# Optimization experiments

Hardware: AMD Instinct MI355X
Metric: run time of the kernel (lower is better)

The kernel has to match this reference:

```python
import jax, jax.numpy as jnp
import numpy as np

B, L, D, DIN, A, V, R = 1024, 100, 256, 704, 128, 32000, 129


def setup_inputs() -> dict:
    key = jax.random.key(0)
    ks = jax.random.split(key, 18)
    s = 0.05
    inp = {
        "x": jax.random.normal(ks[0], (B, DIN), jnp.float32),
        "h0": jax.random.normal(ks[1], (B, D), jnp.float32),
        "c0": jax.random.normal(ks[2], (B, D), jnp.float32),
        "src_enc": jax.random.normal(ks[3], (B, L, D), jnp.float32),
        "src_token_ids": jax.random.randint(ks[4], (B, L), 0, V),
        "W_ih": jax.random.normal(ks[5], (4 * D, DIN), jnp.float32) * s,
        "b_ih": jax.random.normal(ks[6], (4 * D,), jnp.float32) * s,
        "W_hh": jax.random.normal(ks[7], (4 * D, D), jnp.float32) * s,
        "b_hh": jax.random.normal(ks[8], (4 * D,), jnp.float32) * s,
        "W_attn": jax.random.normal(ks[9], (D, D), jnp.float32) * s,
        "W_att_vec": jax.random.normal(ks[10], (A * 2, 2 * D), jnp.float32) * s,
        "W_ptr": jax.random.normal(ks[11], (D, D), jnp.float32) * s,
        "rule_emb": jax.random.normal(ks[12], (R, 128), jnp.float32) * s,
        "W_rule_proj": jax.random.normal(ks[13], (D, 128), jnp.float32) * s,
        "prim_emb": jax.random.normal(ks[14], (V, 128), jnp.float32) * s,
        "W_prim_proj": jax.random.normal(ks[15], (D, 128), jnp.float32) * s,
        "w_gen": jax.random.normal(ks[16], (2, D), jnp.float32) * s,
        "b_gen": jax.random.normal(ks[17], (2,), jnp.float32) * s,
    }
    # W_att_vec maps concat(h, ctx) [2D] -> ATT (=256); keep shape (256, 512)
    inp["W_att_vec"] = inp["W_att_vec"][:256]
    return inp


def reference(x, h0, c0, src_enc, src_token_ids, W_ih, b_ih, W_hh, b_hh,
              W_attn, W_att_vec, W_ptr, rule_emb, W_rule_proj,
              prim_emb, W_prim_proj, w_gen, b_gen):
    # --- LSTMCell (torch gate order i, f, g, o) ---
    gates = x @ W_ih.T + b_ih + h0 @ W_hh.T + b_hh          # [B, 4D]
    i, f, g, o = jnp.split(gates, 4, axis=-1)
    i, f, o = jax.nn.sigmoid(i), jax.nn.sigmoid(f), jax.nn.sigmoid(o)
    c = f * c0 + i * jnp.tanh(g)
    h = o * jnp.tanh(c)                                      # [B, D]

    # --- dot-product attention over source encodings ---
    enc_proj = src_enc @ W_attn.T                            # [B, L, D]
    scores = jnp.einsum('bd,bld->bl', h, enc_proj)
    alpha = jax.nn.softmax(scores, axis=-1)
    ctx = jnp.einsum('bl,bld->bd', alpha, src_enc)
    att = jnp.tanh(jnp.concatenate([h, ctx], axis=-1) @ W_att_vec.T)  # [B, 256]

    # --- apply-rule (production) readout ---
    rule_proj = rule_emb @ W_rule_proj.T                     # [R, 256]
    log_p_rule = jax.nn.log_softmax(att @ rule_proj.T, axis=-1)  # [B, R]

    # --- primitive generation readout ---
    prim_proj = prim_emb @ W_prim_proj.T                     # [V, 256]
    p_gen_prim = jax.nn.softmax(att @ prim_proj.T, axis=-1)  # [B, V]

    # --- pointer network copy distribution over source positions ---
    ptr_scores = jnp.einsum('bld,bd->bl', src_enc @ W_ptr.T, att)
    copy_p = jax.nn.softmax(ptr_scores, axis=-1)             # [B, L]

    # --- gen vs copy gate (softmax over 2, per usage in parse()) ---
    gate = jax.nn.softmax(att @ w_gen.T + b_gen, axis=-1)    # [B, 2]

    # --- combined primitive distribution: gen + scattered copy mass ---
    p_prim = gate[:, :1] * p_gen_prim                        # [B, V]
    copy_mass = gate[:, 1:] * copy_p                         # [B, L]
    bidx = jnp.arange(p_prim.shape[0])[:, None]
    p_prim = p_prim.at[bidx, src_token_ids].add(copy_mass)
    return log_p_rule, p_prim, h, c, att
```

## Files before the change

### kernel.cpp

```cpp
#include <hip/hip_runtime.h>
#include <hip/hip_bf16.h>
#include <math.h>

#define NB   1024
#define LL   100
#define DD   256
#define DINN 704
#define VV   32000
#define RR   129
#define KAV  512

typedef float f32x4 __attribute__((ext_vector_type(4)));
typedef float f32x2 __attribute__((ext_vector_type(2)));
typedef short s16x8 __attribute__((ext_vector_type(8)));
typedef unsigned short u16;

__device__ __forceinline__ float sigf(float x) { return 1.0f / (1.0f + __expf(-x)); }

__device__ __forceinline__ u16 f2bf(float f) {
    unsigned int u = __float_as_uint(f);
    u += 0x7fffu + ((u >> 16) & 1u);
    return (u16)(u >> 16);
}

__global__ __launch_bounds__(256) void k_lstm(
    const float* __restrict__ x, const float* __restrict__ h0, const float* __restrict__ c0,
    const float* __restrict__ W_ih, const float* __restrict__ b_ih,
    const float* __restrict__ W_hh, const float* __restrict__ b_hh,
    float* __restrict__ out_h, float* __restrict__ out_c)
{
    __shared__ __align__(16) float As[16][36];
    __shared__ __align__(16) float Bs[16][68];
    __shared__ __align__(16) float gsm[32][68];
    const int t = threadIdx.x;
    const int row0 = blockIdx.x * 32;
    const int dg = blockIdx.y;
    const int tr = t >> 4, tc = t & 15;
    float acc[2][4] = {};

    for (int kt = 0; kt < 60; ++kt) {
        const float* __restrict__ Asrc;
        const float* __restrict__ Bsrc;
        int lda, kb;
        if (kt < 44) { Asrc = x;  Bsrc = W_ih; lda = DINN; kb = kt * 16; }
        else         { Asrc = h0; Bsrc = W_hh; lda = DD;   kb = (kt - 44) * 16; }
        __syncthreads();
#pragma unroll
        for (int p = 0; p < 2; ++p) {
            int e = t + p * 256;
            int r = e >> 4, kk = e & 15;
            As[kk][r] = Asrc[(row0 + r) * lda + kb + kk];
        }
#pragma unroll
        for (int p = 0; p < 4; ++p) {
            int e = t + p * 256;
            int r = e >> 4, kk = e & 15;
            int n = ((r >> 4) << 8) + dg * 16 + (r & 15);
            Bs[kk][r] = Bsrc[n * lda + kb + kk];
        }
        __syncthreads();
#pragma unroll
        for (int kk = 0; kk < 16; ++kk) {
            float a0 = As[kk][tr * 2], a1 = As[kk][tr * 2 + 1];
            f32x4 b = *reinterpret_cast<const f32x4*>(&Bs[kk][tc * 4]);
#pragma unroll
            for (int i = 0; i < 4; ++i) {
                acc[0][i] = fmaf(a0, b[i], acc[0][i]);
                acc[1][i] = fmaf(a1, b[i], acc[1][i]);
            }
        }
    }
    __syncthreads();
#pragma unroll
    for (int j = 0; j < 2; ++j)
#pragma unroll
        for (int i = 0; i < 4; ++i)
            gsm[tr * 2 + j][tc * 4 + i] = acc[j][i];
    __syncthreads();

#pragma unroll
    for (int p = 0; p < 2; ++p) {
        int item = t + p * 256;
        int r = item >> 4, di = item & 15;
        int dcol = dg * 16 + di;
        float iv = gsm[r][di]      + b_ih[dcol]          + b_hh[dcol];
        float fv = gsm[r][16 + di] + b_ih[DD + dcol]     + b_hh[DD + dcol];
        float gv = gsm[r][32 + di] + b_ih[2 * DD + dcol] + b_hh[2 * DD + dcol];
        float ov = gsm[r][48 + di] + b_ih[3 * DD + dcol] + b_hh[3 * DD + dcol];
        float cprev = c0[(row0 + r) * DD + dcol];
        float cc = sigf(fv) * cprev + sigf(iv) * tanhf(gv);
        float hh = sigf(ov) * tanhf(cc);
        out_c[(row0 + r) * DD + dcol] = cc;
        out_h[(row0 + r) * DD + dcol] = hh;
    }
}

__global__ __launch_bounds__(256) void k_conv(
    const float* __restrict__ src, u16* __restrict__ dst,
    const float* __restrict__ rule_emb, const float* __restrict__ W_rule_proj,
    float* __restrict__ rule_proj,
    const float* __restrict__ W_att_vec, float* __restrict__ wt)
{
    __shared__ float re_s[128];
    __shared__ __align__(16) float tile[64][65];
    const int bx = blockIdx.x, t = threadIdx.x;

    if (bx >= 2000) {
        const int id = bx - 2000;
        const int c0 = (id >> 3) * 64;
        const int k0 = (id & 7) * 64;
        const int r = t >> 6, cc = t & 63;
#pragma unroll
        for (int p = 0; p < 16; ++p)
            tile[r + p * 4][cc] = W_att_vec[(c0 + r + p * 4) * KAV + k0 + cc];
        __syncthreads();
#pragma unroll
        for (int p = 0; p < 16; ++p)
            wt[(k0 + r + p * 4) * DD + c0 + cc] = tile[cc][r + p * 4];
        return;
    }

    if (bx < RR && t < 128) re_s[t] = rule_emb[bx * 128 + t];

    int i = (bx * 256 + t) * 8;
    f32x4 a = *reinterpret_cast<const f32x4*>(&src[i]);
    f32x4 b = *reinterpret_cast<const f32x4*>(&src[i + 4]);
    s16x8 r;
    r[0] = (short)f2bf(a[0]); r[1] = (short)f2bf(a[1]);
    r[2] = (short)f2bf(a[2]); r[3] = (short)f2bf(a[3]);
    r[4] = (short)f2bf(b[0]); r[5] = (short)f2bf(b[1]);
    r[6] = (short)f2bf(b[2]); r[7] = (short)f2bf(b[3]);
    *reinterpret_cast<s16x8*>(&dst[i]) = r;

    if (bx < RR) {
        __syncthreads();
        float acc = 0.f;
        const float* __restrict__ wr = &W_rule_proj[t * 128];
#pragma unroll 8
        for (int k = 0; k < 128; k += 4) {
            f32x4 w4 = *reinterpret_cast<const f32x4*>(&wr[k]);
            acc += w4[0] * re_s[k] + w4[1] * re_s[k + 1]
                 + w4[2] * re_s[k + 2] + w4[3] * re_s[k + 3];
        }
        rule_proj[bx * DD + t] = acc;
    }
}

__global__ __launch_bounds__(256) void k_fused(
    const float* __restrict__ src_enc, const float* __restrict__ h,
    const float* __restrict__ W_attn, const float* __restrict__ Wt,
    const float* __restrict__ rule_proj, const float* __restrict__ W_ptr,
    const float* __restrict__ W_prim_proj, const float* __restrict__ w_gen,
    const float* __restrict__ b_gen,
    float* __restrict__ att_out, float* __restrict__ log_p_rule,
    u16* __restrict__ att_bf, float* __restrict__ gate0_ws,
    float* __restrict__ copy_mass)
{
    __shared__ __align__(16) float hc_s[2 * DD];
    __shared__ __align__(16) float att_s[DD];
    __shared__ __align__(16) float part[4][DD];
    __shared__ __align__(16) float partp[4][128];
    __shared__ float sc_s[LL];
    __shared__ float al_s[LL];
    __shared__ float red_s[RR];
    __shared__ float gl_s[2];
    __shared__ float mS[2];

    const int b = blockIdx.x, t = threadIdx.x;
    const int lane = t & 63, w = t >> 6;
    const float* __restrict__ enc = src_enc + (size_t)b * LL * DD;

    hc_s[t] = h[b * DD + t];
    __syncthreads();

    {
        f32x4 p = {0.f, 0.f, 0.f, 0.f};
        const int e0 = w * 64;
#pragma unroll 4
        for (int e = e0; e < e0 + 64; ++e) {
            float hv = hc_s[e];
            f32x4 wv = *reinterpret_cast<const f32x4*>(&W_attn[e * DD + lane * 4]);
            p[0] = fmaf(hv, wv[0], p[0]); p[1] = fmaf(hv, wv[1], p[1]);
            p[2] = fmaf(hv, wv[2], p[2]); p[3] = fmaf(hv, wv[3], p[3]);
        }
        *reinterpret_cast<f32x4*>(&part[w][lane * 4]) = p;
    }
    __syncthreads();
    f32x4 hw4;
    {
        f32x4 p0 = *reinterpret_cast<const f32x4*>(&part[0][lane * 4]);
        f32x4 p1 = *reinterpret_cast<const f32x4*>(&part[1][lane * 4]);
        f32x4 p2 = *reinterpret_cast<const f32x4*>(&part[2][lane * 4]);
        f32x4 p3 = *reinterpret_cast<const f32x4*>(&part[3][lane * 4]);
        hw4[0] = (p0[0] + p1[0]) + (p2[0] + p3[0]);
        hw4[1] = (p0[1] + p1[1]) + (p2[1] + p3[1]);
        hw4[2] = (p0[2] + p1[2]) + (p2[2] + p3[2]);
        hw4[3] = (p0[3] + p1[3]) + (p2[3] + p3[3]);
    }

    for (int l = w; l < LL; l += 4) {
        f32x4 ev = *reinterpret_cast<const f32x4*>(&enc[l * DD + lane * 4]);
        float pr = hw4[0] * ev[0] + hw4[1] * ev[1] + hw4[2] * ev[2] + hw4[3] * ev[3];
#pragma unroll
        for (int m = 1; m < 64; m <<= 1) pr += __shfl_xor(pr, m);
        if (lane == 0) sc_s[l] = pr;
    }
    __syncthreads();
    if (w == 0) {
        float v0 = sc_s[lane];
        float v1 = (lane + 64 < LL) ? sc_s[lane + 64] : -1e30f;
        float m = fmaxf(v0, v1);
#pragma unroll
        for (int s = 1; s < 64; s <<= 1) m = fmaxf(m, __shfl_xor(m, s));
        float e0 = __expf(v0 - m);
        float e1 = (lane + 64 < LL) ? __expf(v1 - m) : 0.f;
        float ssum = e0 + e1;
#pragma unroll
        for (int s = 1; s < 64; s <<= 1) ssum += __shfl_xor(ssum, s);
        float inv = 1.f / ssum;
        al_s[lane] = e0 * inv;
        if (lane + 64 < LL) al_s[lane + 64] = e1 * inv;
    }
    __syncthreads();

    {
        float a0 = 0.f, a1 = 0.f, a2 = 0.f, a3 = 0.f;
        for (int l = 0; l < LL; l += 4) {
            a0 = fmaf(al_s[l],     enc[(l)     * DD + t], a0);
            a1 = fmaf(al_s[l + 1], enc[(l + 1) * DD + t], a1);
            a2 = fmaf(al_s[l + 2], enc[(l + 2) * DD + t], a2);
            a3 = fmaf(al_s[l + 3], enc[(l + 3) * DD + t], a3);
        }
        hc_s[DD + t] = (a0 + a1) + (a2 + a3);
    }
    __syncthreads();

    {
        f32x4 p = {0.f, 0.f, 0.f, 0.f};
        const int gk0 = w * 128;
#pragma unroll 4
        for (int kk = 0; kk < 128; ++kk) {
            float cv = hc_s[gk0 + kk];
            f32x4 wv = *reinterpret_cast<const f32x4*>(&Wt[(gk0 + kk) * DD + lane * 4]);
            p[0] = fmaf(cv, wv[0], p[0]); p[1] = fmaf(cv, wv[1], p[1]);
            p[2] = fmaf(cv, wv[2], p[2]); p[3] = fmaf(cv, wv[3], p[3]);
        }
        *reinterpret_cast<f32x4*>(&part[w][lane * 4]) = p;
    }
    __syncthreads();
    {
        float av = (part[0][t] + part[1][t]) + (part[2][t] + part[3][t]);
        av = tanhf(av);
        att_s[t] = av;
        att_out[b * DD + t] = av;
    }
    __syncthreads();

    {
        f32x4 p = {0.f, 0.f, 0.f, 0.f};
        const int e0 = w * 64;
#pragma unroll 4
        for (int e = e0; e < e0 + 64; ++e) {
            float av = att_s[e];
            f32x4 wv = *reinterpret_cast<const f32x4*>(&W_ptr[e * DD + lane * 4]);
            p[0] = fmaf(av, wv[0], p[0]); p[1] = fmaf(av, wv[1], p[1]);
            p[2] = fmaf(av, wv[2], p[2]); p[3] = fmaf(av, wv[3], p[3]);
        }
        *reinterpret_cast<f32x4*>(&part[w][lane * 4]) = p;
    }
    {
        float p0 = 0.f, p1 = 0.f;
        const int e0 = w * 64;
#pragma unroll 4
        for (int e = e0; e < e0 + 64; ++e) {
            float av = att_s[e];
            f32x2 wv = *reinterpret_cast<const f32x2*>(&W_prim_proj[e * 128 + lane * 2]);
            p0 = fmaf(av, wv[0], p0);
            p1 = fmaf(av, wv[1], p1);
        }
        partp[w][lane * 2]     = p0;
        partp[w][lane * 2 + 1] = p1;
    }
    if (t < RR) {
        float acc = 0.f;
        const float* __restrict__ rp = &rule_proj[t * DD];
#pragma unroll 4
        for (int d = 0; d < DD; d += 4) {
            f32x4 r4 = *reinterpret_cast<const f32x4*>(&rp[d]);
            f32x4 a4 = *reinterpret_cast<const f32x4*>(&att_s[d]);
            acc += r4[0] * a4[0] + r4[1] * a4[1] + r4[2] * a4[2] + r4[3] * a4[3];
        }
        red_s[t] = acc;
    }
    if (w < 2) {
        f32x4 a4 = *reinterpret_cast<const f32x4*>(&att_s[lane * 4]);
        f32x4 g4 = *reinterpret_cast<const f32x4*>(&w_gen[w * DD + lane * 4]);
        float p = a4[0] * g4[0] + a4[1] * g4[1] + a4[2] * g4[2] + a4[3] * g4[3];
#pragma unroll
        for (int s = 1; s < 64; s <<= 1) p += __shfl_xor(p, s);
        if (lane == 0) gl_s[w] = p + b_gen[w];
    }
    __syncthreads();

    f32x4 aw4;
    {
        f32x4 p0 = *reinterpret_cast<const f32x4*>(&part[0][lane * 4]);
        f32x4 p1 = *reinterpret_cast<const f32x4*>(&part[1][lane * 4]);
        f32x4 p2 = *reinterpret_cast<const f32x4*>(&part[2][lane * 4]);
        f32x4 p3 = *reinterpret_cast<const f32x4*>(&part[3][lane * 4]);
        aw4[0] = (p0[0] + p1[0]) + (p2[0] + p3[0]);
        aw4[1] = (p0[1] + p1[1]) + (p2[1] + p3[1]);
        aw4[2] = (p0[2] + p1[2]) + (p2[2] + p3[2]);
        aw4[3] = (p0[3] + p1[3]) + (p2[3] + p3[3]);
    }
    if (t < 128) {
        float ap = (partp[0][t] + partp[1][t]) + (partp[2][t] + partp[3][t]);
        att_bf[b * 128 + t] = f2bf(ap);
    }
    if (w == 0) {
        float v0 = red_s[lane];
        float v1 = red_s[lane + 64];
        float v2 = (lane == 0) ? red_s[128] : -1e30f;
        float m = fmaxf(fmaxf(v0, v1), v2);
#pragma unroll
        for (int s = 1; s < 64; s <<= 1) m = fmaxf(m, __shfl_xor(m, s));
        float ssum = __expf(v0 - m) + __expf(v1 - m) + ((lane == 0) ? __expf(v2 - m) : 0.f);
#pragma unroll
        for (int s = 1; s < 64; s <<= 1) ssum += __shfl_xor(ssum, s);
        if (lane == 0) { mS[0] = m; mS[1] = logf(ssum); }
    }
    __syncthreads();
    if (t < RR) log_p_rule[b * RR + t] = red_s[t] - mS[0] - mS[1];

    float g0 = gl_s[0], g1 = gl_s[1];
    float gm = fmaxf(g0, g1);
    float e0g = __expf(g0 - gm), e1g = __expf(g1 - gm);
    float gate1 = e1g / (e0g + e1g);
    if (t == 0) gate0_ws[b] = e0g / (e0g + e1g);

    for (int l = w; l < LL; l += 4) {
        f32x4 ev = *reinterpret_cast<const f32x4*>(&enc[l * DD + lane * 4]);
        float pr = aw4[0] * ev[0] + aw4[1] * ev[1] + aw4[2] * ev[2] + aw4[3] * ev[3];
#pragma unroll
        for (int m = 1; m < 64; m <<= 1) pr += __shfl_xor(pr, m);
        if (lane == 0) sc_s[l] = pr;
    }
    __syncthreads();
    if (w == 0) {
        float v0 = sc_s[lane];
        float v1 = (lane + 64 < LL) ? sc_s[lane + 64] : -1e30f;
        float m = fmaxf(v0, v1);
#pragma unroll
        for (int s = 1; s < 64; s <<= 1) m = fmaxf(m, __shfl_xor(m, s));
        float ee0 = __expf(v0 - m);
        float ee1 = (lane + 64 < LL) ? __expf(v1 - m) : 0.f;
        float ssum = ee0 + ee1;
#pragma unroll
        for (int s = 1; s < 64; s <<= 1) ssum += __shfl_xor(ssum, s);
        float inv = 1.f / ssum;
        copy_mass[b * LL + lane] = gate1 * ee0 * inv;
        if (lane + 64 < LL) copy_mass[b * LL + lane + 64] = gate1 * ee1 * inv;
    }
}

template <int PASS>
__global__ __launch_bounds__(256) void k_prim(
    const u16* __restrict__ att_bf, const u16* __restrict__ prim_bf,
    const float* __restrict__ coef, float* __restrict__ stats, float* __restrict__ p_prim)
{
    const int t = threadIdx.x;
    const int lane = t & 63, w = t >> 6;
    const int lm = lane & 15, lq = lane >> 4;
    const int colbase = blockIdx.x * 128 + (w & 1) * 64;
    const int chunk = colbase >> 6;
    const int rowblk = blockIdx.y * 256;

    s16x8 pfr[4][4];
#pragma unroll
    for (int kg = 0; kg < 4; ++kg)
#pragma unroll
        for (int mg = 0; mg < 4; ++mg)
            pfr[kg][mg] = *reinterpret_cast<const s16x8*>(
                &prim_bf[(size_t)(colbase + mg * 16 + lm) * 128 + kg * 32 + lq * 8]);

    for (int it = 0; it < 2; ++it) {
        const int rowbase = rowblk + it * 128 + (w >> 1) * 64;
        f32x4 acc[4][4] = {};
#pragma unroll
        for (int kg = 0; kg < 4; ++kg) {
            s16x8 afr[4];
#pragma unroll
            for (int ng = 0; ng < 4; ++ng)
                afr[ng] = *reinterpret_cast<const s16x8*>(
                    &att_bf[(rowbase + ng * 16 + lm) * 128 + kg * 32 + lq * 8]);
#pragma unroll
            for (int mg = 0; mg < 4; ++mg)
#pragma unroll
                for (int ng = 0; ng < 4; ++ng)
                    acc[mg][ng] = __builtin_amdgcn_mfma_f32_16x16x32_bf16(
                        pfr[kg][mg], afr[ng], acc[mg][ng], 0, 0, 0);
        }
        if (PASS == 0) {
#pragma unroll
            for (int ng = 0; ng < 4; ++ng) {
                float se = 0.f;
#pragma unroll
                for (int mg = 0; mg < 4; ++mg)
                    se += __expf(acc[mg][ng][0]) + __expf(acc[mg][ng][1])
                        + __expf(acc[mg][ng][2]) + __expf(acc[mg][ng][3]);
                se += __shfl_xor(se, 16);
                se += __shfl_xor(se, 32);
                if (lq == 0)
                    stats[chunk * NB + rowbase + ng * 16 + lm] = se;
            }
        } else {
#pragma unroll
            for (int ng = 0; ng < 4; ++ng) {
                const int arow = rowbase + ng * 16 + lm;
                const float cf = coef[arow];
                float* __restrict__ dst = &p_prim[(size_t)arow * VV + colbase + lq * 4];
#pragma unroll
                for (int mg = 0; mg < 4; ++mg) {
                    f32x4 v;
                    v[0] = cf * __expf(acc[mg][ng][0]);
                    v[1] = cf * __expf(acc[mg][ng][1]);
                    v[2] = cf * __expf(acc[mg][ng][2]);
                    v[3] = cf * __expf(acc[mg][ng][3]);
                    *reinterpret_cast<f32x4*>(&dst[mg * 16]) = v;
                }
            }
        }
    }
}

__global__ __launch_bounds__(256) void k_combine(
    const float* __restrict__ stats, const float* __restrict__ gate0_ws,
    float* __restrict__ coef)
{
    const int row = blockIdx.x * 256 + threadIdx.x;
    float s0 = 0.f, s1 = 0.f, s2 = 0.f, s3 = 0.f;
    for (int c = 0; c < 500; c += 4) {
        s0 += stats[(c)     * NB + row];
        s1 += stats[(c + 1) * NB + row];
        s2 += stats[(c + 2) * NB + row];
        s3 += stats[(c + 3) * NB + row];
    }
    coef[row] = gate0_ws[row] / ((s0 + s1) + (s2 + s3));
}

__global__ __launch_bounds__(256) void k_scatter(
    const int* __restrict__ tok, const float* __restrict__ copy_mass, float* __restrict__ p_prim)
{
    int i = blockIdx.x * 256 + threadIdx.x;
    if (i >= NB * LL) return;
    int b = i / LL;
    atomicAdd(&p_prim[(size_t)b * VV + tok[i]], copy_mass[i]);
}

extern "C" void kernel_launch(void* const* d_in, const int* in_sizes, int n_in,
                              void* d_out, int out_size, void* d_ws, size_t ws_size,
                              hipStream_t stream)
{
    const float* x         = (const float*)d_in[0];
    const float* h0        = (const float*)d_in[1];
    const float* c0        = (const float*)d_in[2];
    const float* src_enc   = (const float*)d_in[3];
    const int*   tok       = (const int*)  d_in[4];
    const float* W_ih      = (const float*)d_in[5];
    const float* b_ih      = (const float*)d_in[6];
    const float* W_hh      = (const float*)d_in[7];
    const float* b_hh      = (const float*)d_in[8];
    const float* W_attn    = (const float*)d_in[9];
    const float* W_att_vec = (const float*)d_in[10];
    const float* W_ptr     = (const float*)d_in[11];
    const float* rule_emb  = (const float*)d_in[12];
    const float* W_rule_pr = (const float*)d_in[13];
    const float* prim_emb  = (const float*)d_in[14];
    const float* W_prim_pr = (const float*)d_in[15];
    const float* w_gen     = (const float*)d_in[16];
    const float* b_gen     = (const float*)d_in[17];

    float* out    = (float*)d_out;
    float* o_logp = out;
    float* o_pp   = out + 1024 * 129;
    float* o_h    = o_pp + (size_t)1024 * 32000;
    float* o_c    = o_h + 1024 * 256;
    float* o_att  = o_c + 1024 * 256;

    float* wsf      = (float*)d_ws;
    float* ws_rp    = wsf;
    float* ws_gate  = ws_rp    + 33280;
    float* ws_cm    = ws_gate  + 1024;
    float* ws_coef  = ws_cm    + 102400;
    float* ws_stats = ws_coef  + 1024;
    float* ws_wt    = ws_stats + 512000;
    u16*   ws_attbf = (u16*)(ws_wt + 131072);
    u16*   ws_primbf= (u16*)(ws_wt + 131072 + 65536);

    k_conv<<<dim3(2032), 256, 0, stream>>>(prim_emb, ws_primbf, rule_emb, W_rule_pr,
                                           ws_rp, W_att_vec, ws_wt);
    k_lstm<<<dim3(32, 16), 256, 0, stream>>>(x, h0, c0, W_ih, b_ih, W_hh, b_hh, o_h, o_c);
    k_fused<<<dim3(1024), 256, 0, stream>>>(src_enc, o_h, W_attn, ws_wt, ws_rp, W_ptr,
                                            W_prim_pr, w_gen, b_gen,
                                            o_att, o_logp, ws_attbf, ws_gate, ws_cm);
    k_prim<0><<<dim3(250, 4), 256, 0, stream>>>(ws_attbf, ws_primbf, nullptr, ws_stats, nullptr);
    k_combine<<<dim3(4), 256, 0, stream>>>(ws_stats, ws_gate, ws_coef);
    k_prim<1><<<dim3(250, 4), 256, 0, stream>>>(ws_attbf, ws_primbf, ws_coef, nullptr, o_pp);
    k_scatter<<<dim3(400), 256, 0, stream>>>(tok, ws_cm, o_pp);
}
```

Measured before the change: 249.8 us.

## Stage source encodings once in LDS as bf16 and reuse across attention passes

Each block now loads its row's src_enc slice once, converts it to bf16 and stores it in a padded shared-memory tile. The attention-score, context and pointer-score passes read from that tile instead of re-reading global memory three times, and score computation switches from per-row wave reductions to per-thread dot products. This cuts global memory traffic in a bandwidth-bound kernel, at the cost of bf16 precision on the encoder values and a much larger LDS footprint that lowers occupancy.

```diff
diff --git a/kernel.cpp b/kernel.cpp
--- a/kernel.cpp
+++ b/kernel.cpp
@@ -9,18 +9,23 @@
 #define VV   32000
 #define RR   129
 #define KAV  512
+#define ROWU 129
 
 typedef float f32x4 __attribute__((ext_vector_type(4)));
 typedef float f32x2 __attribute__((ext_vector_type(2)));
 typedef short s16x8 __attribute__((ext_vector_type(8)));
 typedef unsigned short u16;
+typedef unsigned int u32;
 
 __device__ __forceinline__ float sigf(float x) { return 1.0f / (1.0f + __expf(-x)); }
 
 __device__ __forceinline__ u16 f2bf(float f) {
-    unsigned int u = __float_as_uint(f);
+    u32 u = __float_as_uint(f);
     u += 0x7fffu + ((u >> 16) & 1u);
     return (u16)(u >> 16);
+}
+__device__ __forceinline__ float bf2f(u16 s) {
+    return __uint_as_float(((u32)s) << 16);
 }
 
 __global__ __launch_bounds__(256) void k_lstm(
@@ -156,10 +161,11 @@
     u16* __restrict__ att_bf, float* __restrict__ gate0_ws,
     float* __restrict__ copy_mass)
 {
-    __shared__ __align__(16) float hc_s[2 * DD];
-    __shared__ __align__(16) float att_s[DD];
+    __shared__ u32 enc_u[LL * ROWU];
     __shared__ __align__(16) float part[4][DD];
     __shared__ __align__(16) float partp[4][128];
+    __shared__ __align__(16) float hc_s[2 * DD];
+    __shared__ __align__(16) float hw_s[DD];
     __shared__ float sc_s[LL];
     __shared__ float al_s[LL];
     __shared__ float red_s[RR];
@@ -171,6 +177,17 @@
     const float* __restrict__ enc = src_enc + (size_t)b * LL * DD;
 
     hc_s[t] = h[b * DD + t];
+
+#pragma unroll 5
+    for (int p = 0; p < 25; ++p) {
+        int q = p * 256 + t;
+        int l = q >> 6, dq = q & 63;
+        f32x4 ev = *reinterpret_cast<const f32x4*>(&enc[l * DD + dq * 4]);
+        u32 w0 = (u32)f2bf(ev[0]) | ((u32)f2bf(ev[1]) << 16);
+        u32 w1 = (u32)f2bf(ev[2]) | ((u32)f2bf(ev[3]) << 16);
+        enc_u[l * ROWU + dq * 2]     = w0;
+        enc_u[l * ROWU + dq * 2 + 1] = w1;
+    }
     __syncthreads();
 
     {
@@ -186,26 +203,28 @@
         *reinterpret_cast<f32x4*>(&part[w][lane * 4]) = p;
     }
     __syncthreads();
-    f32x4 hw4;
-    {
-        f32x4 p0 = *reinterpret_cast<const f32x4*>(&part[0][lane * 4]);
-        f32x4 p1 = *reinterpret_cast<const f32x4*>(&part[1][lane * 4]);
-        f32x4 p2 = *reinterpret_cast<const f32x4*>(&part[2][lane * 4]);
-        f32x4 p3 = *reinterpret_cast<const f32x4*>(&part[3][lane * 4]);
-        hw4[0] = (p0[0] + p1[0]) + (p2[0] + p3[0]);
-        hw4[1] = (p0[1] + p1[1]) + (p2[1] + p3[1]);
-        hw4[2] = (p0[2] + p1[2]) + (p2[2] + p3[2]);
-        hw4[3] = (p0[3] + p1[3]) + (p2[3] + p3[3]);
-    }
-
-    for (int l = w; l < LL; l += 4) {
-        f32x4 ev = *reinterpret_cast<const f32x4*>(&enc[l * DD + lane * 4]);
-        float pr = hw4[0] * ev[0] + hw4[1] * ev[1] + hw4[2] * ev[2] + hw4[3] * ev[3];
-#pragma unroll
-        for (int m = 1; m < 64; m <<= 1) pr += __shfl_xor(pr, m);
-        if (lane == 0) sc_s[l] = pr;
-    }
-    __syncthreads();
+    hw_s[t] = (part[0][t] + part[1][t]) + (part[2][t] + part[3][t]);
+    __syncthreads();
+
+    {
+        const int sl = ((w >> 1) << 6) + lane;
+        float sp = 0.f;
+        if (sl < LL) {
+            const u32* __restrict__ rp = enc_u + sl * ROWU + ((w & 1) << 6);
+            const float* __restrict__ hp = hw_s + ((w & 1) << 7);
+#pragma unroll 16
+            for (int k = 0; k < 64; ++k) {
+                u32 v = rp[k];
+                sp = fmaf(bf2f((u16)v),         hp[2 * k],     sp);
+                sp = fmaf(bf2f((u16)(v >> 16)), hp[2 * k + 1], sp);
+            }
+        }
+        part[w][lane] = sp;
+    }
+    __syncthreads();
+    if (t < LL) sc_s[t] = part[(t >> 6) << 1][t & 63] + part[((t >> 6) << 1) + 1][t & 63];
+    __syncthreads();
+
     if (w == 0) {
         float v0 = sc_s[lane];
         float v1 = (lane + 64 < LL) ? sc_s[lane + 64] : -1e30f;
@@ -224,15 +243,24 @@
     __syncthreads();
 
     {
-        float a0 = 0.f, a1 = 0.f, a2 = 0.f, a3 = 0.f;
-        for (int l = 0; l < LL; l += 4) {
-            a0 = fmaf(al_s[l],     enc[(l)     * DD + t], a0);
-            a1 = fmaf(al_s[l + 1], enc[(l + 1) * DD + t], a1);
-            a2 = fmaf(al_s[l + 2], enc[(l + 2) * DD + t], a2);
-            a3 = fmaf(al_s[l + 3], enc[(l + 3) * DD + t], a3);
-        }
-        hc_s[DD + t] = (a0 + a1) + (a2 + a3);
-    }
+        const int l0 = w * 25;
+        float c0 = 0.f, c1 = 0.f, c2 = 0.f, c3 = 0.f;
+#pragma unroll 5
+        for (int li = 0; li < 25; ++li) {
+            int l = l0 + li;
+            float a = al_s[l];
+            u32 v0 = enc_u[l * ROWU + lane * 2];
+            u32 v1 = enc_u[l * ROWU + lane * 2 + 1];
+            c0 = fmaf(a, bf2f((u16)v0), c0);
+            c1 = fmaf(a, bf2f((u16)(v0 >> 16)), c1);
+            c2 = fmaf(a, bf2f((u16)v1), c2);
+            c3 = fmaf(a, bf2f((u16)(v1 >> 16)), c3);
+        }
+        f32x4 p; p[0] = c0; p[1] = c1; p[2] = c2; p[3] = c3;
+        *reinterpret_cast<f32x4*>(&part[w][lane * 4]) = p;
+    }
+    __syncthreads();
+    hc_s[DD + t] = (part[0][t] + part[1][t]) + (part[2][t] + part[3][t]);
     __syncthreads();
 
     {
@@ -248,12 +276,10 @@
         *reinterpret_cast<f32x4*>(&part[w][lane * 4]) = p;
     }
     __syncthreads();
-    {
-        float av = (part[0][t] + part[1][t]) + (part[2][t] + part[3][t]);
-        av = tanhf(av);
-        att_s[t] = av;
-        att_out[b * DD + t] = av;
-    }
+    float att_v = tanhf((part[0][t] + part[1][t]) + (part[2][t] + part[3][t]));
+    att_out[b * DD + t] = att_v;
+    __syncthreads();
+    hc_s[t] = att_v;
     __syncthreads();
 
     {
@@ -261,7 +287,7 @@
         const int e0 = w * 64;
 #pragma unroll 4
         for (int e = e0; e < e0 + 64; ++e) {
-            float av = att_s[e];
+            float av = hc_s[e];
             f32x4 wv = *reinterpret_cast<const f32x4*>(&W_ptr[e * DD + lane * 4]);
             p[0] = fmaf(av, wv[0], p[0]); p[1] = fmaf(av, wv[1], p[1]);
             p[2] = fmaf(av, wv[2], p[2]); p[3] = fmaf(av, wv[3], p[3]);
@@ -273,7 +299,7 @@
         const int e0 = w * 64;
 #pragma unroll 4
         for (int e = e0; e < e0 + 64; ++e) {
-            float av = att_s[e];
+            float av = hc_s[e];
             f32x2 wv = *reinterpret_cast<const f32x2*>(&W_prim_proj[e * 128 + lane * 2]);
             p0 = fmaf(av, wv[0], p0);
             p1 = fmaf(av, wv[1], p1);
@@ -287,13 +313,13 @@
 #pragma unroll 4
         for (int d = 0; d < DD; d += 4) {
             f32x4 r4 = *reinterpret_cast<const f32x4*>(&rp[d]);
-            f32x4 a4 = *reinterpret_cast<const f32x4*>(&att_s[d]);
+            f32x4 a4 = *reinterpret_cast<const f32x4*>(&hc_s[d]);
             acc += r4[0] * a4[0] + r4[1] * a4[1] + r4[2] * a4[2] + r4[3] * a4[3];
         }
         red_s[t] = acc;
     }
     if (w < 2) {
-        f32x4 a4 = *reinterpret_cast<const f32x4*>(&att_s[lane * 4]);
+        f32x4 a4 = *reinterpret_cast<const f32x4*>(&hc_s[lane * 4]);
         f32x4 g4 = *reinterpret_cast<const f32x4*>(&w_gen[w * DD + lane * 4]);
         float p = a4[0] * g4[0] + a4[1] * g4[1] + a4[2] * g4[2] + a4[3] * g4[3];
 #pragma unroll
@@ -302,17 +328,7 @@
     }
     __syncthreads();
 
-    f32x4 aw4;
-    {
-        f32x4 p0 = *reinterpret_cast<const f32x4*>(&part[0][lane * 4]);
-        f32x4 p1 = *reinterpret_cast<const f32x4*>(&part[1][lane * 4]);
-        f32x4 p2 = *reinterpret_cast<const f32x4*>(&part[2][lane * 4]);
-        f32x4 p3 = *reinterpret_cast<const f32x4*>(&part[3][lane * 4]);
-        aw4[0] = (p0[0] + p1[0]) + (p2[0] + p3[0]);
-        aw4[1] = (p0[1] + p1[1]) + (p2[1] + p3[1]);
-        aw4[2] = (p0[2] + p1[2]) + (p2[2] + p3[2]);
-        aw4[3] = (p0[3] + p1[3]) + (p2[3] + p3[3]);
-    }
+    hc_s[DD + t] = (part[0][t] + part[1][t]) + (part[2][t] + part[3][t]);
     if (t < 128) {
         float ap = (partp[0][t] + partp[1][t]) + (partp[2][t] + partp[3][t]);
         att_bf[b * 128 + t] = f2bf(ap);
@@ -338,13 +354,23 @@
     float gate1 = e1g / (e0g + e1g);
     if (t == 0) gate0_ws[b] = e0g / (e0g + e1g);
 
-    for (int l = w; l < LL; l += 4) {
-        f32x4 ev = *reinterpret_cast<const f32x4*>(&enc[l * DD + lane * 4]);
-        float pr = aw4[0] * ev[0] + aw4[1] * ev[1] + aw4[2] * ev[2] + aw4[3] * ev[3];
-#pragma unroll
-        for (int m = 1; m < 64; m <<= 1) pr += __shfl_xor(pr, m);
-        if (lane == 0) sc_s[l] = pr;
-    }
+    {
+        const int sl = ((w >> 1) << 6) + lane;
+        float sp = 0.f;
+        if (sl < LL) {
+            const u32* __restrict__ rp = enc_u + sl * ROWU + ((w & 1) << 6);
+            const float* __restrict__ ap = hc_s + DD + ((w & 1) << 7);
+#pragma unroll 16
+            for (int k = 0; k < 64; ++k) {
+                u32 v = rp[k];
+                sp = fmaf(bf2f((u16)v),         ap[2 * k],     sp);
+                sp = fmaf(bf2f((u16)(v >> 16)), ap[2 * k + 1], sp);
+            }
+        }
+        part[w][lane] = sp;
+    }
+    __syncthreads();
+    if (t < LL) sc_s[t] = part[(t >> 6) << 1][t & 63] + part[((t >> 6) << 1) + 1][t & 63];
     __syncthreads();
     if (w == 0) {
         float v0 = sc_s[lane];
```

Result: faster. 240.7 us (-3.6%).
